# Kernel optimization log

Measured on AMD Instinct MI355X. Metric: run time of the kernel, lower is better.

The kernel has to match this reference:

```python
import jax, jax.numpy as jnp
import numpy as np

B, S, D, H, NL = 4, 1024, 512, 8, 2
DFF = 4 * D
EPS = 1e-5


def _layernorm(x, g, b):
    m = x.mean(-1, keepdims=True)
    v = ((x - m) ** 2).mean(-1, keepdims=True)
    return (x - m) / jnp.sqrt(v + EPS) * g + b


def _forward(x, Wq, bq, Wk, bk, Wv, bv, Wo, bo, W1, b1, W2, b2, ln1_g, ln1_b, ln2_g, ln2_b):
    Bn, Sn, Dn = x.shape
    Nl, Hh = Wq.shape[0], Wq.shape[1]
    dk = Dn // Hh  # scaling uses dmodel//h even though heads are full-width (faithful to SDPA)
    for i in range(Nl):
        # per-head full-width projections: each head maps dmodel -> dmodel
        q = jnp.einsum('bsd,hed->bhse', x, Wq[i]) + bq[i][:, None, :]
        k = jnp.einsum('bsd,hed->bhse', x, Wk[i]) + bk[i][:, None, :]
        v = jnp.einsum('bsd,hed->bhse', x, Wv[i]) + bv[i][:, None, :]
        scores = jnp.einsum('bhse,bhte->bhst', q, k) / jnp.sqrt(jnp.asarray(dk, x.dtype))
        attn = jax.nn.softmax(scores, axis=-1)
        heads = jnp.einsum('bhst,bhte->bhse', attn, v)          # [B,H,S,D]
        cat = heads.transpose(0, 2, 1, 3).reshape(Bn, Sn, Hh * Dn)  # concat heads -> [B,S,H*D]
        mha_out = cat @ Wo[i].T + bo[i]
        x = _layernorm(x + mha_out, ln1_g[i], ln1_b[i])
        ff = jax.nn.relu(x @ W1[i].T + b1[i]) @ W2[i].T + b2[i]
        x = _layernorm(x + ff, ln2_g[i], ln2_b[i])
    return x


def setup_inputs() -> dict:
    key = jax.random.key(0)
    ks = jax.random.split(key, 12)
    def w(k, shape, fan_in):
        return (jax.random.normal(k, shape, jnp.float32) / np.sqrt(fan_in)).astype(jnp.float32)
    inp = {
        'x': jax.random.normal(ks[0], (B, S, D), jnp.float32),
        'Wq': w(ks[1], (NL, H, D, D), D), 'bq': jnp.zeros((NL, H, D), jnp.float32),
        'Wk': w(ks[2], (NL, H, D, D), D), 'bk': jnp.zeros((NL, H, D), jnp.float32),
        'Wv': w(ks[3], (NL, H, D, D), D), 'bv': jnp.zeros((NL, H, D), jnp.float32),
        'Wo': w(ks[4], (NL, D, H * D), H * D), 'bo': jnp.zeros((NL, D), jnp.float32),
        'W1': w(ks[5], (NL, DFF, D), D), 'b1': jnp.zeros((NL, DFF), jnp.float32),
        'W2': w(ks[6], (NL, D, DFF), DFF), 'b2': jnp.zeros((NL, D), jnp.float32),
        'ln1_g': jnp.ones((NL, D), jnp.float32), 'ln1_b': jnp.zeros((NL, D), jnp.float32),
        'ln2_g': jnp.ones((NL, D), jnp.float32), 'ln2_b': jnp.zeros((NL, D), jnp.float32),
    }
    return inp


def reference(x, Wq, bq, Wk, bk, Wv, bv, Wo, bo, W1, b1, W2, b2, ln1_g, ln1_b, ln2_g, ln2_b):
    return _forward(x, Wq, bq, Wk, bk, Wv, bv, Wo, bo, W1, b1, W2, b2, ln1_g, ln1_b, ln2_g, ln2_b)
```

## Files before the change

### kernel.cpp

```cpp
#include <hip/hip_runtime.h>
#include <cstdint>
#include <cstddef>

#define NB 4
#define NS 1024
#define ND 512
#define NH 8
#define NLAYER 2
#define NDFF 2048

typedef __attribute__((ext_vector_type(8))) short short8;
typedef __attribute__((ext_vector_type(4))) float f32x4;
typedef __attribute__((ext_vector_type(4))) unsigned short u16x4;
typedef unsigned short u16;
typedef long long ll;

__device__ __forceinline__ float b2f(u16 u) {
  union { unsigned int i; float f; } x; x.i = ((unsigned int)u) << 16; return x.f;
}
__device__ __forceinline__ u16 f2b(float f) {
  union { float f; unsigned int i; } x; x.f = f;
  return (u16)((x.i + 0x7FFF + ((x.i >> 16) & 1)) >> 16);
}

struct Zm { int div; ll hi, lo; };
__device__ __forceinline__ ll zoff(Zm m, int z) {
  return (ll)(z / m.div) * m.hi + (ll)(z % m.div) * m.lo;
}

enum { F_BF16 = 1, F_RELU = 2, F_BCOL = 4, F_BROW = 8, F_RESID = 16 };

__device__ __forceinline__ void load_lds16(const void* g, void* s) {
  __builtin_amdgcn_global_load_lds(
      (const __attribute__((address_space(1))) void*)(uintptr_t)g,
      (__attribute__((address_space(3))) void*)(uint32_t)(uintptr_t)s, 16, 0, 0);
}

#define MFMA16(d, a, b) \
  asm volatile("v_mfma_f32_16x16x32_bf16 %0, %1, %2, %0" : "+v"(d) : "v"(a), "v"(b))

__global__ void __launch_bounds__(256)
gemm_bt(const u16* __restrict__ A, int lda, Zm za,
        const u16* __restrict__ Bw, int ldb, Zm zb,
        const u16* __restrict__ Bw2, const float* __restrict__ bias2, int zsplit,
        void* __restrict__ Cv, int ldc, Zm zc,
        const float* __restrict__ bias, Zm zbias,
        const float* __restrict__ resid,
        float scale, int K, int flags)
{
  __shared__ __align__(16) char smem[2][16384];

  const int gx = gridDim.x, gy = gridDim.y;
  int id = (blockIdx.z * gy + blockIdx.y) * gx + blockIdx.x;
  const int nwg = gx * gy * (int)gridDim.z;
  if ((nwg & 7) == 0) id = (id & 7) * (nwg >> 3) + (id >> 3);
  const int bx = id % gx;
  const int rest = id / gx;
  const int by = rest % gy;
  const int z0 = rest / gy;

  int zB = z0;
  const u16* Bsel = Bw;
  const float* bsel = bias;
  if (z0 >= zsplit) { Bsel = Bw2; bsel = bias2; zB = z0 - zsplit; }

  A    += zoff(za, z0);
  Bsel += zoff(zb, zB);

  const int bm = by * 128, bn = bx * 128;
  const int t = threadIdx.x;
  const int w = t >> 6, lane = t & 63;
  const int wr = w >> 1, wc = w & 1;

  const u16* ga0 = A    + (size_t)(bm + (t >> 2)) * lda + ((t & 3) << 3);
  const u16* ga1 = ga0 + (size_t)64 * lda;
  const u16* gb0 = Bsel + (size_t)(bn + (t >> 2)) * ldb + ((t & 3) << 3);
  const u16* gb1 = gb0 + (size_t)64 * ldb;

  auto STAGE = [&](int sel, int kt) {
    const int k0 = kt << 5;
    char* sa = smem[sel] + (w << 10);
    char* sb = smem[sel] + 8192 + (w << 10);
    load_lds16(ga0 + k0, sa);
    load_lds16(ga1 + k0, sa + 4096);
    load_lds16(gb0 + k0, sb);
    load_lds16(gb1 + k0, sb + 4096);
  };

  f32x4 acc[4][4];
#pragma unroll
  for (int i = 0; i < 4; ++i)
#pragma unroll
    for (int j = 0; j < 4; ++j) acc[i][j] = (f32x4){0.f, 0.f, 0.f, 0.f};

  const int fr = lane & 15;
  const int kg = (lane >> 4) << 3;

  const int nt = K >> 5;
  STAGE(0, 0);
  __syncthreads();
  int cur = 0;
  for (int kt = 0; kt < nt; ++kt) {
    if (kt + 1 < nt) STAGE(cur ^ 1, kt + 1);
    const u16* la = (const u16*)smem[cur];
    const u16* lb = (const u16*)(smem[cur] + 8192);
    short8 af[4], bf[4];
#pragma unroll
    for (int mi = 0; mi < 4; ++mi)
      af[mi] = *(const short8*)(la + (wr * 64 + mi * 16 + fr) * 32 + kg);
#pragma unroll
    for (int ni = 0; ni < 4; ++ni)
      bf[ni] = *(const short8*)(lb + (wc * 64 + ni * 16 + fr) * 32 + kg);
#pragma unroll
    for (int mi = 0; mi < 4; ++mi)
#pragma unroll
      for (int ni = 0; ni < 4; ++ni)
        MFMA16(acc[mi][ni], af[mi], bf[ni]);
    __syncthreads();
    cur ^= 1;
  }

  asm volatile("s_nop 7\n\ts_nop 7" ::: "memory");

  const ll co = zoff(zc, z0);
  const float* bz = (flags & (F_BCOL | F_BROW)) ? bsel + zoff(zbias, zB) : nullptr;
  const int r0 = (lane >> 4) << 2;
  const int c0 = lane & 15;
#pragma unroll
  for (int mi = 0; mi < 4; ++mi) {
#pragma unroll
    for (int ni = 0; ni < 4; ++ni) {
#pragma unroll
      for (int r = 0; r < 4; ++r) {
        const int grow = bm + wr * 64 + mi * 16 + r0 + r;
        const int gcol = bn + wc * 64 + ni * 16 + c0;
        float v = acc[mi][ni][r] * scale;
        if (flags & F_BCOL) v += bz[gcol];
        if (flags & F_BROW) v += bz[grow];
        if (flags & F_RELU) v = fmaxf(v, 0.f);
        if (flags & F_RESID) v += resid[(size_t)grow * ldc + gcol];
        const ll idx = co + (ll)grow * ldc + gcol;
        if (flags & F_BF16) ((u16*)Cv)[idx] = f2b(v);
        else                ((float*)Cv)[idx] = v;
      }
    }
  }
}

__global__ void __launch_bounds__(256, 2)
fattn(const u16* __restrict__ qg, const u16* __restrict__ kg,
      const u16* __restrict__ vtg, u16* __restrict__ cat)
{
  __shared__ __align__(16) u16 qk_lds[192 * 128];
  __shared__ __align__(16) u16 p_lds[64 * 136];

  int id = blockIdx.x;
  id = (id & 7) * 64 + (id >> 3);
  const int qt = id & 15;
  const int hb = id >> 4;
  const int h = hb >> 2, b = hb & 3;

  const ll hbase = (ll)h * NB * NS * ND;
  const u16* Q  = qg  + hbase + ((ll)(b * NS + qt * 64)) * ND;
  const u16* Kp = kg  + hbase + (ll)b * NS * ND;
  const u16* VT = vtg + (ll)hb * ND * NS;
  u16* Op = cat + ((ll)(b * NS + qt * 64)) * (NH * ND) + h * ND;

  const int t = threadIdx.x;
  const int w = t >> 6, lane = t & 63;
  const int fr = lane & 15, khi = lane >> 4;

  const int srow = t >> 4;
  const int scol = (((t & 15) ^ (srow & 7)) << 3);
  char* const qkb = (char*)qk_lds;
  const int wslab = w << 10;

  f32x4 o[4][8];
#pragma unroll
  for (int ec = 0; ec < 4; ++ec)
#pragma unroll
    for (int nf = 0; nf < 8; ++nf) o[ec][nf] = (f32x4){0.f, 0.f, 0.f, 0.f};
  float m_r[4] = {-1e30f, -1e30f, -1e30f, -1e30f};
  float l_r[4] = {0.f, 0.f, 0.f, 0.f};

  for (int kv = 0; kv < 8; ++kv) {
    f32x4 s[8];
#pragma unroll
    for (int nf = 0; nf < 8; ++nf) s[nf] = (f32x4){0.f, 0.f, 0.f, 0.f};

    for (int dch = 0; dch < 4; ++dch) {
#pragma unroll
      for (int i = 0; i < 4; ++i)
        load_lds16(Q + (ll)(i * 16 + srow) * ND + dch * 128 + scol,
                   qkb + i * 4096 + wslab);
#pragma unroll
      for (int i = 0; i < 8; ++i)
        load_lds16(Kp + (ll)(kv * 128 + i * 16 + srow) * ND + dch * 128 + scol,
                   qkb + 16384 + i * 4096 + wslab);
      __syncthreads();
#pragma unroll
      for (int ks = 0; ks < 4; ++ks) {
        const int gq = (((4 * ks + khi) ^ (fr & 7)) << 3);
        short8 aq = *(const short8*)(qk_lds + (w * 16 + fr) * 128 + gq);
#pragma unroll
        for (int nf = 0; nf < 8; ++nf) {
          short8 bk = *(const short8*)(qk_lds + 8192 + (nf * 16 + fr) * 128 + gq);
          MFMA16(s[nf], aq, bk);
        }
      }
      __syncthreads();
    }
    asm volatile("s_nop 7\n\ts_nop 7" ::: "memory");

#pragma unroll
    for (int r = 0; r < 4; ++r) {
      float v[8];
#pragma unroll
      for (int nf = 0; nf < 8; ++nf) v[nf] = s[nf][r] * 0.125f;
      float mx = v[0];
#pragma unroll
      for (int nf = 1; nf < 8; ++nf) mx = fmaxf(mx, v[nf]);
      mx = fmaxf(mx, __shfl_xor(mx, 1));
      mx = fmaxf(mx, __shfl_xor(mx, 2));
      mx = fmaxf(mx, __shfl_xor(mx, 4));
      mx = fmaxf(mx, __shfl_xor(mx, 8));
      const float mn = fmaxf(m_r[r], mx);
      const float f = __expf(m_r[r] - mn);
      m_r[r] = mn;
      float sum = 0.f;
#pragma unroll
      for (int nf = 0; nf < 8; ++nf) { v[nf] = __expf(v[nf] - mn); sum += v[nf]; }
      sum += __shfl_xor(sum, 1);
      sum += __shfl_xor(sum, 2);
      sum += __shfl_xor(sum, 4);
      sum += __shfl_xor(sum, 8);
      l_r[r] = l_r[r] * f + sum;
#pragma unroll
      for (int nf = 0; nf < 8; ++nf)
        p_lds[(w * 16 + 4 * khi + r) * 136 + nf * 16 + fr] = f2b(v[nf]);
#pragma unroll
      for (int ec = 0; ec < 4; ++ec)
#pragma unroll
        for (int nf = 0; nf < 8; ++nf) o[ec][nf][r] *= f;
    }

#pragma unroll
    for (int ec = 0; ec < 4; ++ec) {
#pragma unroll
      for (int i = 0; i < 8; ++i)
        load_lds16(VT + (ll)(ec * 128 + i * 16 + srow) * NS + kv * 128 + scol,
                   qkb + i * 4096 + wslab);
      __syncthreads();
#pragma unroll
      for (int ks = 0; ks < 4; ++ks) {
        short8 ap = *(const short8*)(p_lds + (w * 16 + fr) * 136 + 32 * ks + 8 * khi);
        const int gv = (((4 * ks + khi) ^ (fr & 7)) << 3);
#pragma unroll
        for (int nf = 0; nf < 8; ++nf) {
          short8 bv8 = *(const short8*)(qk_lds + (nf * 16 + fr) * 128 + gv);
          MFMA16(o[ec][nf], ap, bv8);
        }
      }
      __syncthreads();
    }
  }

  asm volatile("s_nop 7\n\ts_nop 7" ::: "memory");
#pragma unroll
  for (int r = 0; r < 4; ++r) {
    const float inv = 1.f / l_r[r];
    const ll row = (ll)(w * 16 + 4 * khi + r) * (NH * ND);
#pragma unroll
    for (int ec = 0; ec < 4; ++ec)
#pragma unroll
      for (int nf = 0; nf < 8; ++nf)
        Op[row + ec * 128 + nf * 16 + fr] = f2b(o[ec][nf][r] * inv);
  }
}

__global__ void __launch_bounds__(256)
ln_red(const float* __restrict__ parts, int np, ll pstride,
       const float* __restrict__ bias, const float* __restrict__ resid,
       const float* __restrict__ g, const float* __restrict__ be,
       float* __restrict__ xout, u16* __restrict__ xbout)
{
  const int t = threadIdx.x, w = t >> 6, lane = t & 63;
  const ll row = (ll)blockIdx.x * 4 + w;
  const ll base = row * ND + lane * 8;
  float v[8];
  *(f32x4*)(v)     = *(const f32x4*)(resid + base);
  *(f32x4*)(v + 4) = *(const f32x4*)(resid + base + 4);
#pragma unroll
  for (int j = 0; j < 8; ++j) v[j] += bias[lane * 8 + j];
  for (int pIdx = 0; pIdx < np; ++pIdx) {
    const float* pp = parts + pIdx * pstride + base;
    f32x4 a0 = *(const f32x4*)(pp);
    f32x4 a1 = *(const f32x4*)(pp + 4);
    v[0] += a0.x; v[1] += a0.y; v[2] += a0.z; v[3] += a0.w;
    v[4] += a1.x; v[5] += a1.y; v[6] += a1.z; v[7] += a1.w;
  }
  float s = 0.f, q = 0.f;
#pragma unroll
  for (int j = 0; j < 8; ++j) { s += v[j]; q += v[j] * v[j]; }
#pragma unroll
  for (int o = 32; o >= 1; o >>= 1) { s += __shfl_xor(s, o); q += __shfl_xor(q, o); }
  const float mean = s * (1.f / ND);
  const float var  = q * (1.f / ND) - mean * mean;
  const float inv  = 1.f / sqrtf(var + 1e-5f);
#pragma unroll
  for (int j = 0; j < 8; ++j) {
    const int c = lane * 8 + j;
    const float y = (v[j] - mean) * inv * g[c] + be[c];
    xout[row * ND + c] = y;
    xbout[row * ND + c] = f2b(y);
  }
}

struct CvtJobs { const float* src[7]; u16* dst[7]; ll n[7]; };

__global__ void __launch_bounds__(256)
cvt7(CvtJobs j)
{
  const int z = blockIdx.y;
  const ll i = ((ll)blockIdx.x * 256 + threadIdx.x) * 4;
  if (i >= j.n[z]) return;
  f32x4 v = *(const f32x4*)(j.src[z] + i);
  u16x4 o;
  o.x = f2b(v.x); o.y = f2b(v.y); o.z = f2b(v.z); o.w = f2b(v.w);
  *(u16x4*)(j.dst[z] + i) = o;
}

extern "C" void kernel_launch(void* const* d_in, const int* in_sizes, int n_in,
                              void* d_out, int out_size, void* d_ws, size_t ws_size,
                              hipStream_t stream)
{
  (void)in_sizes; (void)n_in; (void)out_size; (void)ws_size;
  const float* x_in = (const float*)d_in[0];
  const float* Wq = (const float*)d_in[1];  const float* bq = (const float*)d_in[2];
  const float* Wk = (const float*)d_in[3];  const float* bk = (const float*)d_in[4];
  const float* Wv = (const float*)d_in[5];  const float* bv = (const float*)d_in[6];
  const float* Wo = (const float*)d_in[7];  const float* bo = (const float*)d_in[8];
  const float* W1 = (const float*)d_in[9];  const float* b1 = (const float*)d_in[10];
  const float* W2 = (const float*)d_in[11]; const float* b2 = (const float*)d_in[12];
  const float* ln1g = (const float*)d_in[13]; const float* ln1b = (const float*)d_in[14];
  const float* ln2g = (const float*)d_in[15]; const float* ln2b = (const float*)d_in[16];

  char* p = (char*)d_ws;
  auto alloc = [&](ll bytes) { char* r = p; p += (bytes + 255) & ~(ll)255; return r; };
  const ll nWq = (ll)NLAYER * NH * ND * ND;
  const ll nWo = (ll)NLAYER * ND * NH * ND;
  const ll nW1 = (ll)NLAYER * NDFF * ND;
  const ll nX  = (ll)NB * NS * ND;

  u16* wq_b = (u16*)alloc(nWq * 2);
  u16* wk_b = (u16*)alloc(nWq * 2);
  u16* wv_b = (u16*)alloc(nWq * 2);
  u16* wo_b = (u16*)alloc(nWo * 2);
  u16* w1_b = (u16*)alloc(nW1 * 2);
  u16* w2_b = (u16*)alloc(nW1 * 2);
  u16* xb   = (u16*)alloc(nX * 2);
  u16* qb   = (u16*)alloc((ll)NH * NB * NS * ND * 2);
  u16* kb   = (u16*)alloc((ll)NH * NB * NS * ND * 2);
  u16* vT   = (u16*)alloc((ll)NH * NB * ND * NS * 2);
  u16* scb  = (u16*)alloc((ll)NB * NH * NS * NS * 2);
  u16* cat = scb;
  float* parts = (float*)(scb + (ll)NB * NS * NH * ND);
  u16* ffh = qb;

  CvtJobs cj;
  cj.src[0] = Wq; cj.dst[0] = wq_b; cj.n[0] = nWq;
  cj.src[1] = Wk; cj.dst[1] = wk_b; cj.n[1] = nWq;
  cj.src[2] = Wv; cj.dst[2] = wv_b; cj.n[2] = nWq;
  cj.src[3] = Wo; cj.dst[3] = wo_b; cj.n[3] = nWo;
  cj.src[4] = W1; cj.dst[4] = w1_b; cj.n[4] = nW1;
  cj.src[5] = W2; cj.dst[5] = w2_b; cj.n[5] = nW1;
  cj.src[6] = x_in; cj.dst[6] = xb; cj.n[6] = nX;
  cvt7<<<dim3((unsigned)((nWq / 4 + 255) / 256), 7), 256, 0, stream>>>(cj);

  float* xf = (float*)d_out;
  const Zm Z0{1, 0, 0};
  const ll PSTR = nX;
  const int ZINF = 1 << 30;

  for (int i = 0; i < NLAYER; ++i) {
    const float* resid1 = (i == 0) ? x_in : xf;
    const ll woff = (ll)i * NH * ND * ND;

    gemm_bt<<<dim3(ND/128, (NB*NS)/128, 2*NH), 256, 0, stream>>>(
        xb, ND, Z0,
        wq_b + woff, ND, Zm{1, (ll)ND * ND, 0},
        wk_b + woff, bk + (ll)i * NH * ND, NH,
        qb, ND, Zm{1, (ll)NB * NS * ND, 0},
        bq + (ll)i * NH * ND, Zm{1, ND, 0}, nullptr, 1.f, ND, F_BF16 | F_BCOL);

    gemm_bt<<<dim3(NS/128, ND/128, NH*NB), 256, 0, stream>>>(
        wv_b + woff, ND, Zm{NB, (ll)ND * ND, 0},
        xb, ND, Zm{NB, 0, (ll)NS * ND},
        xb, nullptr, ZINF,
        vT, NS, Zm{1, (ll)ND * NS, 0},
        bv + (ll)i * NH * ND, Zm{NB, ND, 0}, nullptr, 1.f, ND, F_BF16 | F_BROW);

    fattn<<<dim3(512), 256, 0, stream>>>(qb, kb, vT, cat);

    gemm_bt<<<dim3(ND/128, (NB*NS)/128, 4), 256, 0, stream>>>(
        cat, NH * ND, Zm{1, 1024, 0},
        wo_b + (ll)i * ND * NH * ND, NH * ND, Zm{1, 1024, 0},
        wo_b, nullptr, ZINF,
        parts, ND, Zm{1, PSTR, 0},
        nullptr, Z0, nullptr, 1.f, 1024, 0);

    ln_red<<<dim3(NB * NS / 4), 256, 0, stream>>>(
        parts, 4, PSTR, bo + (ll)i * ND, resid1,
        ln1g + (ll)i * ND, ln1b + (ll)i * ND, xf, xb);

    gemm_bt<<<dim3(NDFF/128, (NB*NS)/128, 1), 256, 0, stream>>>(
        xb, ND, Z0,
        w1_b + (ll)i * NDFF * ND, ND, Z0,
        w1_b, nullptr, ZINF,
        ffh, NDFF, Z0,
        b1 + (ll)i * NDFF, Z0, nullptr, 1.f, ND, F_BF16 | F_BCOL | F_RELU);

    gemm_bt<<<dim3(ND/128, (NB*NS)/128, 4), 256, 0, stream>>>(
        ffh, NDFF, Zm{1, 512, 0},
        w2_b + (ll)i * ND * NDFF, NDFF, Zm{1, 512, 0},
        w2_b, nullptr, ZINF,
        parts, ND, Zm{1, PSTR, 0},
        nullptr, Z0, nullptr, 1.f, 512, 0);

    ln_red<<<dim3(NB * NS / 4), 256, 0, stream>>>(
        parts, 4, PSTR, b2 + (ll)i * ND, xf,
        ln2g + (ll)i * ND, ln2b + (ll)i * ND, xf, xb);
  }
}
```

Measured before the change: 685.0 us.

## Double-buffer K/V staging in flash attention, keep Q in registers, lazy rescale

Restructures the fused attention kernel. Q is held in registers instead of being reloaded into LDS for every KV tile. K and V chunks are staged through a two-slot LDS buffer so the next chunk's async load overlaps the current MFMAs, which halves the barriers per chunk. The KV tile shrinks to 64, with a swizzled P buffer. Output rescaling is skipped unless the running max grows by more than a threshold (FA4-style lazy rescale). The launch-bounds occupancy hint is dropped, and the 64-register Q tile raises register pressure, which may reduce occupancy.

```diff
diff --git a/kernel.cpp b/kernel.cpp
--- a/kernel.cpp
+++ b/kernel.cpp
@@ -147,12 +147,12 @@
   }
 }
 
-__global__ void __launch_bounds__(256, 2)
+__global__ void __launch_bounds__(256)
 fattn(const u16* __restrict__ qg, const u16* __restrict__ kg,
       const u16* __restrict__ vtg, u16* __restrict__ cat)
 {
-  __shared__ __align__(16) u16 qk_lds[192 * 128];
-  __shared__ __align__(16) u16 p_lds[64 * 136];
+  __shared__ __align__(16) u16 stg[2][64 * 128];
+  __shared__ __align__(16) u16 p_lds[64 * 64];
 
   int id = blockIdx.x;
   id = (id & 7) * 64 + (id >> 3);
@@ -161,19 +161,38 @@
   const int h = hb >> 2, b = hb & 3;
 
   const ll hbase = (ll)h * NB * NS * ND;
-  const u16* Q  = qg  + hbase + ((ll)(b * NS + qt * 64)) * ND;
+  const u16* Q  = qg  + hbase + (ll)(b * NS + qt * 64) * ND;
   const u16* Kp = kg  + hbase + (ll)b * NS * ND;
   const u16* VT = vtg + (ll)hb * ND * NS;
-  u16* Op = cat + ((ll)(b * NS + qt * 64)) * (NH * ND) + h * ND;
+  u16* Op = cat + (ll)(b * NS + qt * 64) * (NH * ND) + h * ND;
 
   const int t = threadIdx.x;
   const int w = t >> 6, lane = t & 63;
   const int fr = lane & 15, khi = lane >> 4;
 
-  const int srow = t >> 4;
-  const int scol = (((t & 15) ^ (srow & 7)) << 3);
-  char* const qkb = (char*)qk_lds;
-  const int wslab = w << 10;
+  short8 qreg[16];
+#pragma unroll
+  for (int s = 0; s < 16; ++s)
+    qreg[s] = *(const short8*)(Q + (ll)(w * 16 + fr) * ND + s * 32 + khi * 8);
+
+  const int srowK = t >> 4;
+  const int scolK = (((t & 15) ^ (srowK & 7)) << 3);
+  const int srowV = t >> 3;
+  const int scolV = (((t & 7) ^ (srowV & 7)) << 3);
+  const int wofs = w << 10;
+
+  auto STG_K = [&](int buf, int kv, int dch) {
+#pragma unroll
+    for (int i = 0; i < 4; ++i)
+      load_lds16(Kp + (ll)(kv * 64 + i * 16 + srowK) * ND + dch * 128 + scolK,
+                 (char*)stg[buf] + i * 4096 + wofs);
+  };
+  auto STG_V = [&](int buf, int kv, int ec) {
+#pragma unroll
+    for (int i = 0; i < 4; ++i)
+      load_lds16(VT + (ll)(ec * 128 + i * 32 + srowV) * NS + kv * 64 + scolV,
+                 (char*)stg[buf] + i * 4096 + wofs);
+  };
 
   f32x4 o[4][8];
 #pragma unroll
@@ -183,85 +202,102 @@
   float m_r[4] = {-1e30f, -1e30f, -1e30f, -1e30f};
   float l_r[4] = {0.f, 0.f, 0.f, 0.f};
 
-  for (int kv = 0; kv < 8; ++kv) {
-    f32x4 s[8];
-#pragma unroll
-    for (int nf = 0; nf < 8; ++nf) s[nf] = (f32x4){0.f, 0.f, 0.f, 0.f};
-
+  STG_K(0, 0, 0);
+  __syncthreads();
+  int cur = 0;
+
+  for (int kv = 0; kv < 16; ++kv) {
+    f32x4 s[4];
+#pragma unroll
+    for (int nf = 0; nf < 4; ++nf) s[nf] = (f32x4){0.f, 0.f, 0.f, 0.f};
+
+#pragma unroll
     for (int dch = 0; dch < 4; ++dch) {
-#pragma unroll
-      for (int i = 0; i < 4; ++i)
-        load_lds16(Q + (ll)(i * 16 + srow) * ND + dch * 128 + scol,
-                   qkb + i * 4096 + wslab);
-#pragma unroll
-      for (int i = 0; i < 8; ++i)
-        load_lds16(Kp + (ll)(kv * 128 + i * 16 + srow) * ND + dch * 128 + scol,
-                   qkb + 16384 + i * 4096 + wslab);
-      __syncthreads();
+      if (dch < 3) STG_K(cur ^ 1, kv, dch + 1);
+      else         STG_V(cur ^ 1, kv, 0);
+      const u16* kb_ = stg[cur];
 #pragma unroll
       for (int ks = 0; ks < 4; ++ks) {
-        const int gq = (((4 * ks + khi) ^ (fr & 7)) << 3);
-        short8 aq = *(const short8*)(qk_lds + (w * 16 + fr) * 128 + gq);
-#pragma unroll
-        for (int nf = 0; nf < 8; ++nf) {
-          short8 bk = *(const short8*)(qk_lds + 8192 + (nf * 16 + fr) * 128 + gq);
+        const short8 aq = qreg[dch * 4 + ks];
+#pragma unroll
+        for (int nf = 0; nf < 4; ++nf) {
+          const short8 bk = *(const short8*)(
+              kb_ + (nf * 16 + fr) * 128 + ((((4 * ks + khi)) ^ (fr & 7)) << 3));
           MFMA16(s[nf], aq, bk);
         }
       }
       __syncthreads();
+      cur ^= 1;
     }
     asm volatile("s_nop 7\n\ts_nop 7" ::: "memory");
 
+    float mxs[4];
+    bool big = false;
 #pragma unroll
     for (int r = 0; r < 4; ++r) {
-      float v[8];
-#pragma unroll
-      for (int nf = 0; nf < 8; ++nf) v[nf] = s[nf][r] * 0.125f;
-      float mx = v[0];
-#pragma unroll
-      for (int nf = 1; nf < 8; ++nf) mx = fmaxf(mx, v[nf]);
+      float mx = s[0][r];
+#pragma unroll
+      for (int nf = 1; nf < 4; ++nf) mx = fmaxf(mx, s[nf][r]);
+      mx *= 0.125f;
       mx = fmaxf(mx, __shfl_xor(mx, 1));
       mx = fmaxf(mx, __shfl_xor(mx, 2));
       mx = fmaxf(mx, __shfl_xor(mx, 4));
       mx = fmaxf(mx, __shfl_xor(mx, 8));
-      const float mn = fmaxf(m_r[r], mx);
-      const float f = __expf(m_r[r] - mn);
+      mxs[r] = mx;
+      big = big || (mx > m_r[r] + 8.f);
+    }
+    const bool resc = __any(big);
+    float f_r[4];
+#pragma unroll
+    for (int r = 0; r < 4; ++r) {
+      const float mn = resc ? fmaxf(m_r[r], mxs[r]) : m_r[r];
+      f_r[r] = resc ? __expf(m_r[r] - mn) : 1.f;
       m_r[r] = mn;
       float sum = 0.f;
-#pragma unroll
-      for (int nf = 0; nf < 8; ++nf) { v[nf] = __expf(v[nf] - mn); sum += v[nf]; }
+      const int R = w * 16 + 4 * khi + r;
+#pragma unroll
+      for (int nf = 0; nf < 4; ++nf) {
+        const float e = __expf(s[nf][r] * 0.125f - mn);
+        sum += e;
+        const int g = (nf * 2 + (fr >> 3)) ^ ((4 * khi + r) & 7);
+        p_lds[R * 64 + (g << 3) + (fr & 7)] = f2b(e);
+      }
       sum += __shfl_xor(sum, 1);
       sum += __shfl_xor(sum, 2);
       sum += __shfl_xor(sum, 4);
       sum += __shfl_xor(sum, 8);
-      l_r[r] = l_r[r] * f + sum;
-#pragma unroll
-      for (int nf = 0; nf < 8; ++nf)
-        p_lds[(w * 16 + 4 * khi + r) * 136 + nf * 16 + fr] = f2b(v[nf]);
+      l_r[r] = l_r[r] * f_r[r] + sum;
+    }
+    if (resc) {
 #pragma unroll
       for (int ec = 0; ec < 4; ++ec)
 #pragma unroll
-        for (int nf = 0; nf < 8; ++nf) o[ec][nf][r] *= f;
-    }
+        for (int nf = 0; nf < 8; ++nf)
+#pragma unroll
+          for (int r = 0; r < 4; ++r) o[ec][nf][r] *= f_r[r];
+    }
+
+    short8 ap[2];
+#pragma unroll
+    for (int ks2 = 0; ks2 < 2; ++ks2)
+      ap[ks2] = *(const short8*)(
+          p_lds + (w * 16 + fr) * 64 + ((((4 * ks2 + khi)) ^ (fr & 7)) << 3));
 
 #pragma unroll
     for (int ec = 0; ec < 4; ++ec) {
-#pragma unroll
-      for (int i = 0; i < 8; ++i)
-        load_lds16(VT + (ll)(ec * 128 + i * 16 + srow) * NS + kv * 128 + scol,
-                   qkb + i * 4096 + wslab);
+      if (ec < 3)           STG_V(cur ^ 1, kv, ec + 1);
+      else if (kv < 15)     STG_K(cur ^ 1, kv + 1, 0);
+      const u16* vb = stg[cur];
+#pragma unroll
+      for (int ks2 = 0; ks2 < 2; ++ks2)
+#pragma unroll
+        for (int nf = 0; nf < 8; ++nf) {
+          const short8 bv = *(const short8*)(
+              vb + (nf * 16 + fr) * 64 + ((((4 * ks2 + khi)) ^ (fr & 7)) << 3));
+          MFMA16(o[ec][nf], ap[ks2], bv);
+        }
       __syncthreads();
-#pragma unroll
-      for (int ks = 0; ks < 4; ++ks) {
-        short8 ap = *(const short8*)(p_lds + (w * 16 + fr) * 136 + 32 * ks + 8 * khi);
-        const int gv = (((4 * ks + khi) ^ (fr & 7)) << 3);
-#pragma unroll
-        for (int nf = 0; nf < 8; ++nf) {
-          short8 bv8 = *(const short8*)(qk_lds + (nf * 16 + fr) * 128 + gv);
-          MFMA16(o[ec][nf], ap, bv8);
-        }
-      }
-      __syncthreads();
+      cur ^= 1;
     }
   }
 
```

Result: slower. 783.1 us (+14.3%).
